# Performance work log

Hardware: AMD Instinct MI355X
Metric: run time of the kernel (lower is better)

Reference implementation:

```python
import jax, jax.numpy as jnp
import numpy as np

N_HEAD = 16
D_QK = 128
D_V = 128
D_MODEL = 2048
BATCH = 2
SEQ = 2048


def alibi_slopes(n_head):
    # standard ALiBi slopes: 2^(-8*i/n_head) for i = 1..n_head
    return jnp.asarray(2.0 ** (-8.0 * np.arange(1, n_head + 1) / n_head), dtype=jnp.float32)


def setup_inputs() -> dict:
    key = jax.random.key(0)
    k1, k2, k3, k4, k5 = jax.random.split(key, 5)
    x = jax.random.normal(k1, (BATCH, SEQ, D_MODEL), dtype=jnp.float32)
    # causal attention mask (1 = keep, 0 = masked), broadcast over heads
    causal = jnp.tril(jnp.ones((SEQ, SEQ), dtype=bool))
    attention_mask = jnp.broadcast_to(causal, (BATCH, 1, SEQ, SEQ))
    Wq = jax.random.normal(k2, (D_MODEL, N_HEAD * D_QK), dtype=jnp.float32) * (D_MODEL ** -0.5)
    Wk = jax.random.normal(k3, (D_MODEL, N_HEAD * D_QK), dtype=jnp.float32) * (D_MODEL ** -0.5)
    Wv = jax.random.normal(k4, (D_MODEL, N_HEAD * D_V), dtype=jnp.float32) * (D_MODEL ** -0.5)
    Wo = jax.random.normal(k5, (N_HEAD * D_V, D_MODEL), dtype=jnp.float32) * ((N_HEAD * D_V) ** -0.5)
    return {"x": x, "attention_mask": attention_mask, "Wq": Wq, "Wk": Wk, "Wv": Wv, "Wo": Wo}


def reference(x, attention_mask, Wq, Wk, Wv, Wo):
    B, S, _ = x.shape
    scale = D_QK ** -0.5
    q = (x @ Wq).reshape(B, S, N_HEAD, D_QK).transpose(0, 2, 1, 3)  # [B,H,S,dqk]
    k = (x @ Wk).reshape(B, S, N_HEAD, D_QK).transpose(0, 2, 1, 3)
    v = (x @ Wv).reshape(B, S, N_HEAD, D_V).transpose(0, 2, 1, 3)
    scores = jnp.einsum('bhid,bhjd->bhij', q, k) * scale  # [B,H,S,S]
    # ALiBi bias: slope_h * (j - i), negative penalty for distant past keys
    pos = jnp.arange(S, dtype=jnp.float32)
    rel = pos[None, :] - pos[:, None]  # [S,S]
    slopes = alibi_slopes(N_HEAD)
    scores = scores + slopes[None, :, None, None] * rel[None, None, :, :]
    scores = jnp.where(attention_mask, scores, jnp.float32(-jnp.inf))
    attn = jax.nn.softmax(scores, axis=-1)
    out = jnp.einsum('bhij,bhjd->bhid', attn, v)  # [B,H,S,dv]
    out = out.transpose(0, 2, 1, 3).reshape(B, S, N_HEAD * D_V)
    return out @ Wo
```

## Files before the change

### kernel.cpp

```cpp
#include <hip/hip_runtime.h>
#include <cstdint>

typedef unsigned short u16;
typedef __attribute__((ext_vector_type(4))) u16 u16x4;
typedef __attribute__((ext_vector_type(8))) u16 u16x8;
typedef __attribute__((ext_vector_type(8))) __bf16 bf16x8;
typedef __attribute__((ext_vector_type(4))) float f32x4;

#define LOG2E 1.44269504088896340736f

static __device__ __forceinline__ u16 f2bf(float f) {
  unsigned u = __builtin_bit_cast(unsigned, f);
  u += 0x7fffu + ((u >> 16) & 1u);
  return (u16)(u >> 16);
}
static __device__ __forceinline__ float bf2f(u16 v) {
  unsigned u = ((unsigned)v) << 16;
  return __builtin_bit_cast(float, u);
}


static __device__ __forceinline__ void gload16(const u16* g, u16* l) {
  __builtin_amdgcn_global_load_lds(
      (__attribute__((address_space(1))) void*)(uintptr_t)g,
      (__attribute__((address_space(3))) void*)(uintptr_t)l, 16, 0, 0);
}

static __device__ __forceinline__ bf16x8 lds_bf8(const void* p) {
  return __builtin_bit_cast(bf16x8, *(const u16x8*)p);
}

__global__ __launch_bounds__(256) void cast_x_kernel(const float* __restrict__ src,
                                                     u16* __restrict__ dst) {
  int i = (blockIdx.x * 256 + threadIdx.x) * 4;
  float4 v = *(const float4*)(src + i);
  u16x4 r = {f2bf(v.x), f2bf(v.y), f2bf(v.z), f2bf(v.w)};
  *(u16x4*)(dst + i) = r;
}

__global__ __launch_bounds__(256) void transpose_w4_kernel(const float* Wq, const float* Wk,
                                                           const float* Wv, const float* Wo,
                                                           u16* Wqt, u16* Wkt, u16* Wvt,
                                                           u16* Wot) {
  const float* src = blockIdx.z == 0 ? Wq : (blockIdx.z == 1 ? Wk : (blockIdx.z == 2 ? Wv : Wo));
  u16* dst = blockIdx.z == 0 ? Wqt : (blockIdx.z == 1 ? Wkt : (blockIdx.z == 2 ? Wvt : Wot));
  __shared__ float tile[32][33];
  const int n0 = blockIdx.x * 32, k0 = blockIdx.y * 32;
  const int tx = threadIdx.x & 31, ty = threadIdx.x >> 5;
#pragma unroll
  for (int r = 0; r < 4; ++r) {
    int row = r * 8 + ty;
    tile[row][tx] = src[(size_t)(k0 + row) * 2048 + n0 + tx];
  }
  __syncthreads();
#pragma unroll
  for (int r = 0; r < 4; ++r) {
    int row = r * 8 + ty;
    dst[(size_t)(n0 + row) * 2048 + k0 + tx] = f2bf(tile[tx][row]);
  }
}

#define QSTAGE(TILE, S)                                                              \
  do {                                                                               \
    const int bkq = (TILE) * 64;                                                     \
    u16* as_ = &lds[(S) * 16384];                                                    \
    u16* bs_ = &lds[32768 + (S) * 16384];                                            \
    gload16(pAq + bkq, as_ + tid * 8);                                               \
    gload16(pAq + bkq + (size_t)64 * 2048, as_ + 4096 + tid * 8);                    \
    gload16(pAq + bkq + (size_t)128 * 2048, as_ + 8192 + tid * 8);                   \
    gload16(pAq + bkq + (size_t)192 * 2048, as_ + 12288 + tid * 8);                  \
    gload16(pBq + bkq, bs_ + tid * 8);                                               \
    gload16(pBq + bkq + (size_t)64 * 2048, bs_ + 4096 + tid * 8);                    \
    gload16(pBq + bkq + (size_t)128 * 2048, bs_ + 8192 + tid * 8);                   \
    gload16(pBq + bkq + (size_t)192 * 2048, bs_ + 12288 + tid * 8);                  \
  } while (0)

#define QPH(S, STAGE_STMT)                                                           \
  do {                                                                               \
    const char* as_ = (const char*)&lds[(S) * 16384];                                \
    const char* bs_ = (const char*)&lds[32768 + (S) * 16384];                        \
    bf16x8 af0[8], bq0[4], af1[8], bq1[4];                                           \
    _Pragma("unroll") for (int mf = 0; mf < 8; ++mf) {                               \
      const int ar = wm * 128 + mf * 16 + l16;                                       \
      af0[mf] = lds_bf8(as_ + ((ar * 128 + lg * 16) ^ ((l16 & 7) << 4)));            \
    }                                                                                \
    _Pragma("unroll") for (int nf = 0; nf < 4; ++nf) {                               \
      const int br = wn * 64 + nf * 16 + l16;                                        \
      bq0[nf] = lds_bf8(bs_ + ((br * 128 + lg * 16) ^ ((l16 & 7) << 4)));            \
    }                                                                                \
    STAGE_STMT;                                                                      \
    asm volatile("s_barrier" ::: "memory");                                          \
    __builtin_amdgcn_s_setprio(1);                                                   \
    _Pragma("unroll") for (int mf = 0; mf < 8; ++mf)                                 \
        _Pragma("unroll") for (int nf = 0; nf < 4; ++nf) acc[mf][nf] =               \
            __builtin_amdgcn_mfma_f32_16x16x32_bf16(af0[mf], bq0[nf], acc[mf][nf], 0, 0, 0); \
    _Pragma("unroll") for (int mf = 0; mf < 8; ++mf) {                               \
      const int ar = wm * 128 + mf * 16 + l16;                                       \
      af1[mf] = lds_bf8(as_ + ((ar * 128 + (4 + lg) * 16) ^ ((l16 & 7) << 4)));      \
    }                                                                                \
    _Pragma("unroll") for (int nf = 0; nf < 4; ++nf) {                               \
      const int br = wn * 64 + nf * 16 + l16;                                        \
      bq1[nf] = lds_bf8(bs_ + ((br * 128 + (4 + lg) * 16) ^ ((l16 & 7) << 4)));      \
    }                                                                                \
    _Pragma("unroll") for (int mf = 0; mf < 8; ++mf)                                 \
        _Pragma("unroll") for (int nf = 0; nf < 4; ++nf) acc[mf][nf] =               \
            __builtin_amdgcn_mfma_f32_16x16x32_bf16(af1[mf], bq1[nf], acc[mf][nf], 0, 0, 0); \
    __builtin_amdgcn_s_setprio(0);                                                   \
    __builtin_amdgcn_sched_barrier(0);                                               \
    asm volatile("s_waitcnt vmcnt(0)\n\ts_barrier" ::: "memory");                    \
  } while (0)

__global__ __launch_bounds__(512, 1) void qkproj_kernel(const u16* __restrict__ xb,
                                                        const u16* __restrict__ Wqt,
                                                        const u16* __restrict__ Wkt,
                                                        u16* __restrict__ Qb,
                                                        u16* __restrict__ Kb) {
  const int n0g = blockIdx.y * 256;
  const u16* Bt = (n0g < 2048) ? Wqt : Wkt;
  u16* Cout = (n0g < 2048) ? Qb : Kb;
  const int m0 = blockIdx.x * 256, n0 = n0g & 2047;
  __shared__ u16 lds[65536];
  const int tid = threadIdx.x, lane = tid & 63, w = tid >> 6;
  const int wm = w >> 2, wn = w & 3;
  const int l16 = lane & 15, lg = lane >> 4;
  const int scol2 = ((tid & 7) ^ ((tid >> 3) & 7)) * 8;
  const u16* pAq = xb + (size_t)(m0 + (tid >> 3)) * 2048 + scol2;
  const u16* pBq = Bt + (size_t)(n0 + (tid >> 3)) * 2048 + scol2;

  f32x4 acc[8][4];
#pragma unroll
  for (int i = 0; i < 8; ++i)
#pragma unroll
    for (int j = 0; j < 4; ++j) acc[i][j] = f32x4{0.f, 0.f, 0.f, 0.f};

  QSTAGE(0, 0);
  asm volatile("s_waitcnt vmcnt(0)\n\ts_barrier" ::: "memory");
  for (int t = 0; t < 30; t += 2) {
    QPH(0, QSTAGE(t + 1, 1));
    QPH(1, QSTAGE(t + 2, 0));
  }
  QPH(0, QSTAGE(31, 1));
  QPH(1, (void)0);

#pragma unroll
  for (int mf = 0; mf < 8; ++mf)
#pragma unroll
    for (int nf = 0; nf < 4; ++nf)
#pragma unroll
      for (int r = 0; r < 4; ++r) {
        const int row = m0 + wm * 128 + mf * 16 + lg * 4 + r;
        const int col = n0 + wn * 64 + nf * 16 + l16;
        size_t off =
            (((size_t)(row >> 11) * 16 + (col >> 7)) * 2048 + (row & 2047)) * 128 + (col & 127);
        Cout[off] = f2bf(acc[mf][nf][r]);
      }
}

#define GSTAGE2(TILE, S)                                                             \
  do {                                                                               \
    const int bk2 = (TILE) * 64;                                                     \
    u16* as_ = &lds[(S) * 16384];                                                    \
    u16* bs_ = &lds[49152 + (S) * 8192];                                             \
    gload16(pA2 + bk2, as_ + tid * 8);                                               \
    gload16(pA2 + bk2 + (size_t)64 * 2048, as_ + 4096 + tid * 8);                    \
    gload16(pA2 + bk2 + (size_t)128 * 2048, as_ + 8192 + tid * 8);                   \
    gload16(pA2 + bk2 + (size_t)192 * 2048, as_ + 12288 + tid * 8);                  \
    gload16(pB2 + bk2, bs_ + tid * 8);                                               \
    gload16(pB2 + bk2 + (size_t)64 * 2048, bs_ + 4096 + tid * 8);                    \
  } while (0)

#define GPH2(S, STAGE_STMT, VMLIT)                                                   \
  do {                                                                               \
    const char* as_ = (const char*)&lds[(S) * 16384];                                \
    const char* bs_ = (const char*)&lds[49152 + (S) * 8192];                         \
    bf16x8 af[2][8], bq[2][2];                                                       \
    _Pragma("unroll") for (int kh = 0; kh < 2; ++kh)                                 \
        _Pragma("unroll") for (int mf = 0; mf < 8; ++mf) {                           \
      const int ar = wm * 128 + mf * 16 + l16;                                       \
      af[kh][mf] = lds_bf8(as_ + ((ar * 128 + (kh * 4 + lg) * 16) ^ ((l16 & 7) << 4))); \
    }                                                                                \
    _Pragma("unroll") for (int kh = 0; kh < 2; ++kh)                                 \
        _Pragma("unroll") for (int nf = 0; nf < 2; ++nf) {                           \
      const int br = wn * 32 + nf * 16 + l16;                                        \
      bq[kh][nf] = lds_bf8(bs_ + ((br * 128 + (kh * 4 + lg) * 16) ^ ((l16 & 7) << 4))); \
    }                                                                                \
    STAGE_STMT;                                                                      \
    asm volatile("s_barrier" ::: "memory");                                          \
    __builtin_amdgcn_s_setprio(1);                                                   \
    _Pragma("unroll") for (int kh = 0; kh < 2; ++kh)                                 \
        _Pragma("unroll") for (int mf = 0; mf < 8; ++mf)                             \
            _Pragma("unroll") for (int nf = 0; nf < 2; ++nf) acc[mf][nf] =           \
                __builtin_amdgcn_mfma_f32_16x16x32_bf16(af[kh][mf], bq[kh][nf],      \
                                                        acc[mf][nf], 0, 0, 0);      \
    __builtin_amdgcn_s_setprio(0);                                                   \
    __builtin_amdgcn_sched_barrier(0);                                               \
    asm volatile("s_waitcnt vmcnt(" #VMLIT ")\n\ts_barrier" ::: "memory");           \
  } while (0)

template <int MODE>
__device__ __forceinline__ void gemm_dp2(const u16* __restrict__ A, const u16* __restrict__ Bt,
                                         void* __restrict__ Cout, int m0, int n0) {
  __shared__ u16 lds[73728];
  const int tid = threadIdx.x, lane = tid & 63, w = tid >> 6;
  const int wm = w >> 2, wn = w & 3;
  const int l16 = lane & 15, lg = lane >> 4;
  const int scol2 = ((tid & 7) ^ ((tid >> 3) & 7)) * 8;
  const u16* pA2 = A + (size_t)(m0 + (tid >> 3)) * 2048 + scol2;
  const u16* pB2 = Bt + (size_t)(n0 + (tid >> 3)) * 2048 + scol2;

  f32x4 acc[8][2];
#pragma unroll
  for (int i = 0; i < 8; ++i)
#pragma unroll
    for (int j = 0; j < 2; ++j) acc[i][j] = f32x4{0.f, 0.f, 0.f, 0.f};

  GSTAGE2(0, 0);
  GSTAGE2(1, 1);
  asm volatile("s_waitcnt vmcnt(6)\n\ts_barrier" ::: "memory");
  for (int t = 0; t < 30; t += 3) {
    GPH2(0, GSTAGE2(t + 2, 2), 6);
    GPH2(1, GSTAGE2(t + 3, 0), 6);
    GPH2(2, GSTAGE2(t + 4, 1), 6);
  }
  GPH2(0, (void)0, 0);
  GPH2(1, (void)0, 0);

#pragma unroll
  for (int mf = 0; mf < 8; ++mf)
#pragma unroll
    for (int nf = 0; nf < 2; ++nf)
#pragma unroll
      for (int r = 0; r < 4; ++r) {
        const int row = m0 + wm * 128 + mf * 16 + lg * 4 + r;
        const int col = n0 + wn * 32 + nf * 16 + l16;
        const float v = acc[mf][nf][r];
        if constexpr (MODE == 2) {
          size_t off =
              (((size_t)(col >> 11) * 16 + (row >> 7)) * 128 + (row & 127)) * 2048 + (col & 2047);
          ((u16*)Cout)[off] = f2bf(v);
        } else {
          ((float*)Cout)[(size_t)row * 2048 + col] = v;
        }
      }
}

__global__ __launch_bounds__(512, 1) void vt_kernel(const u16* Wvt, const u16* xb, u16* Vb) {
  gemm_dp2<2>(Wvt, xb, Vb, blockIdx.x * 256, blockIdx.y * 128);
}

__global__ __launch_bounds__(512, 1) void out_kernel(const u16* OA, const u16* Wot, float* C) {
  gemm_dp2<1>(OA, Wot, C, blockIdx.x * 256, blockIdx.y * 128);
}

__global__ __launch_bounds__(256) void attn_kernel(const u16* __restrict__ Q,
                                                   const u16* __restrict__ Kg,
                                                   const u16* __restrict__ Vg,
                                                   u16* __restrict__ O,
                                                   u16* __restrict__ Opart,
                                                   float* __restrict__ Lp) {
  const int tid = threadIdx.x, lane = tid & 63, w = tid >> 6;
  const int l16 = lane & 15, lg = lane >> 4;

  const int u = blockIdx.x >> 5, bh = blockIdx.x & 31;
  int tile, st0, st1, slot = 0;
  bool multi = false;
  if (u == 0) { tile = 17; st0 = 0; st1 = 18; }
  else if (u == 1) { tile = 16; st0 = 0; st1 = 17; }
  else if (u < 30) {
    multi = true;
    const int c = u - 2, ti = c >> 1, ch = c & 1;
    tile = 31 - ti;
    const int s = tile + 1, half = (s + 1) >> 1;
    st0 = ch ? half : 0;
    st1 = ch ? s : half;
    slot = bh * 28 + c;
  } else { tile = 45 - u; st0 = 0; st1 = tile + 1; }

  const int q0 = tile * 64;
  const int h = bh & 15, b = bh >> 4;
  const float sl2 = exp2f(-0.5f * (float)(h + 1)) * LOG2E;
  const float sc2 = 0.08838834764831845f * LOG2E;

  __shared__ u16 Kl[64 * 128];
  __shared__ u16 Vl[128 * 64];
  __shared__ u16 Pl[64 * 64];

  const size_t qk_base = (size_t)bh * 2048 * 128;
  const size_t v_base = (size_t)bh * 128 * 2048;

  const u16* kgs = Kg + qk_base + (size_t)(tid >> 4) * 128 + (((tid & 15) ^ ((tid >> 4) & 7)) * 8);
  const u16* vgs = Vg + v_base + (size_t)(tid >> 3) * 2048 + (((tid & 7) ^ ((tid >> 3) & 7)) * 8);

#define STAGEKV(STX)                                                        \
  do {                                                                      \
    const int j0s = (STX)*64;                                               \
    _Pragma("unroll") for (int s = 0; s < 4; ++s) {                         \
      gload16(kgs + (size_t)(j0s + s * 16) * 128, Kl + s * 2048 + tid * 8); \
      gload16(vgs + (size_t)s * 32 * 2048 + j0s, Vl + s * 2048 + tid * 8);  \
    }                                                                       \
  } while (0)

  STAGEKV(st0);

  bf16x8 qf[4];
#pragma unroll
  for (int ks = 0; ks < 4; ++ks)
    qf[ks] = lds_bf8(&Q[qk_base + (size_t)(q0 + w * 16 + l16) * 128 + ks * 32 + lg * 8]);

  f32x4 oacc[8];
#pragma unroll
  for (int j = 0; j < 8; ++j) oacc[j] = f32x4{0.f, 0.f, 0.f, 0.f};
  float lsum0 = 0.f, lsum1 = 0.f;

  float ab4[4], rsl[4];
#pragma unroll
  for (int nf = 0; nf < 4; ++nf)
    ab4[nf] = (float)(st0 * 64 + nf * 16 - q0 - w * 16 - l16) * sl2;
#pragma unroll
  for (int r = 0; r < 4; ++r) rsl[r] = (float)(lg * 4 + r) * sl2;
  const float abinc = 64.0f * sl2;
  const int qrow = w * 16 + l16;
  const int dmaskb = lg * 4 - w * 16 - l16;

  __syncthreads();

#define ASTEP(MASKED)                                                                     \
  do {                                                                                    \
    f32x4 sacc[4];                                                                        \
    _Pragma("unroll") for (int j = 0; j < 4; ++j) sacc[j] = f32x4{0.f, 0.f, 0.f, 0.f};    \
    __builtin_amdgcn_s_setprio(1);                                                        \
    _Pragma("unroll") for (int ks = 0; ks < 4; ++ks) {                                    \
      bf16x8 kf[4];                                                                       \
      _Pragma("unroll") for (int nf = 0; nf < 4; ++nf) {                                  \
        int j = nf * 16 + l16;                                                            \
        kf[nf] = lds_bf8((char*)Kl + ((j * 256 + (ks * 32 + lg * 8) * 2) ^ ((j & 7) << 4))); \
      }                                                                                   \
      _Pragma("unroll") for (int nf = 0; nf < 4; ++nf) sacc[nf] =                         \
          __builtin_amdgcn_mfma_f32_16x16x32_bf16(kf[nf], qf[ks], sacc[nf], 0, 0, 0);     \
    }                                                                                     \
    __builtin_amdgcn_s_setprio(0);                                                        \
    _Pragma("unroll") for (int nf = 0; nf < 4; ++nf) {                                    \
      float pvv[4];                                                                       \
      _Pragma("unroll") for (int r = 0; r < 4; ++r) {                                     \
        float s2 = fmaf(sacc[nf][r], sc2, ab4[nf] + rsl[r]);                              \
        float pv = exp2f(s2);                                                             \
        if (MASKED) pv = (nf * 16 + r + dmaskb <= 0) ? pv : 0.f;                          \
        pvv[r] = pv;                                                                      \
      }                                                                                   \
      ab4[nf] += abinc;                                                                   \
      lsum0 += pvv[0] + pvv[1];                                                           \
      lsum1 += pvv[2] + pvv[3];                                                           \
      unsigned w0_, w1_;                                                                  \
      asm("v_cvt_pk_bf16_f32 %0, %1, %2" : "=v"(w0_) : "v"(pvv[0]), "v"(pvv[1]));         \
      asm("v_cvt_pk_bf16_f32 %0, %1, %2" : "=v"(w1_) : "v"(pvv[2]), "v"(pvv[3]));         \
      uint2 pw_{w0_, w1_};                                                                \
      *(uint2*)((char*)Pl + ((qrow * 128 + (nf * 16 + lg * 4) * 2) ^ ((qrow & 7) << 4))) = pw_; \
    }                                                                                     \
    __builtin_amdgcn_s_setprio(1);                                                        \
    _Pragma("unroll") for (int ks = 0; ks < 2; ++ks) {                                    \
      bf16x8 pf =                                                                         \
          lds_bf8((char*)Pl + ((qrow * 128 + (ks * 32 + lg * 8) * 2) ^ ((qrow & 7) << 4))); \
      _Pragma("unroll") for (int nf = 0; nf < 8; ++nf) {                                  \
        int d = nf * 16 + l16;                                                            \
        bf16x8 vf =                                                                       \
            lds_bf8((char*)Vl + ((d * 128 + (ks * 32 + lg * 8) * 2) ^ ((d & 7) << 4)));   \
        oacc[nf] = __builtin_amdgcn_mfma_f32_16x16x32_bf16(pf, vf, oacc[nf], 0, 0, 0);    \
      }                                                                                   \
    }                                                                                     \
    __builtin_amdgcn_s_setprio(0);                                                        \
    if (st + 1 < st1) {                                                                   \
      __syncthreads();                                                                    \
      STAGEKV(st + 1);                                                                    \
      __syncthreads();                                                                    \
    }                                                                                     \
  } while (0)

  int st = st0;
  const int bulk_end = min(st1, tile);
  for (; st < bulk_end; ++st) ASTEP(false);
  for (; st < st1; ++st) ASTEP(true);
#undef STAGEKV
#undef ASTEP

  float lr = lsum0 + lsum1;
  lr += __shfl_xor(lr, 16, 64);
  lr += __shfl_xor(lr, 32, 64);

  if (multi) {
    if (lg == 0) Lp[(size_t)slot * 64 + qrow] = lr;
#pragma unroll
    for (int r = 0; r < 4; ++r) {
      const int row = w * 16 + lg * 4 + r;
#pragma unroll
      for (int nf = 0; nf < 8; ++nf)
        Opart[((size_t)slot * 64 + row) * 128 + nf * 16 + l16] = f2bf(oacc[nf][r]);
    }
  } else {
#pragma unroll
    for (int r = 0; r < 4; ++r) {
      const float inv = 1.0f / __shfl(lr, lg * 4 + r, 64);
      const int srow = q0 + w * 16 + lg * 4 + r;
#pragma unroll
      for (int nf = 0; nf < 8; ++nf)
        O[((size_t)b * 2048 + srow) * 2048 + h * 128 + nf * 16 + l16] = f2bf(oacc[nf][r] * inv);
    }
  }
}

__global__ __launch_bounds__(256) void combine_kernel(const u16* __restrict__ Opart,
                                                      const float* __restrict__ Lp,
                                                      u16* __restrict__ O) {
  const int bx = blockIdx.x;
  const int bh = bx / 14, ti = bx % 14;
  const int tile = 31 - ti;
  const int slot0 = bh * 28 + ti * 2, slot1 = slot0 + 1;
  const int b = bh >> 4, h = bh & 15;
  const int q0 = tile * 64;
  const int tid = threadIdx.x;
  const int colg = (tid & 15) * 8, rowb = tid >> 4;
#pragma unroll
  for (int rr = 0; rr < 4; ++rr) {
    const int row = rowb + rr * 16;
    const float l0 = Lp[(size_t)slot0 * 64 + row];
    const float l1 = Lp[(size_t)slot1 * 64 + row];
    const float inv = 1.0f / (l0 + l1);
    u16x8 p0 = *(const u16x8*)&Opart[((size_t)slot0 * 64 + row) * 128 + colg];
    u16x8 p1 = *(const u16x8*)&Opart[((size_t)slot1 * 64 + row) * 128 + colg];
    u16x8 o;
#pragma unroll
    for (int e = 0; e < 8; ++e) o[e] = f2bf((bf2f(p0[e]) + bf2f(p1[e])) * inv);
    *(u16x8*)&O[((size_t)b * 2048 + q0 + row) * 2048 + h * 128 + colg] = o;
  }
}

extern "C" void kernel_launch(void* const* d_in, const int* in_sizes, int n_in, void* d_out,
                              int out_size, void* d_ws, size_t ws_size, hipStream_t stream) {
  const float* x = (const float*)d_in[0];
  const float* Wq = (const float*)d_in[2];
  const float* Wk = (const float*)d_in[3];
  const float* Wv = (const float*)d_in[4];
  const float* Wo = (const float*)d_in[5];
  char* ws = (char*)d_ws;

  const size_t MB = 1048576;
  u16* xb = (u16*)(ws);
  u16* Qb = (u16*)(ws + 16 * MB);
  u16* Kb = (u16*)(ws + 32 * MB);
  u16* Vb = (u16*)(ws + 48 * MB);
  u16* Wqt = (u16*)(ws + 64 * MB);
  u16* Wkt = (u16*)(ws + 72 * MB);
  u16* Wvt = (u16*)(ws + 80 * MB);
  u16* Wot = (u16*)(ws + 88 * MB);
  u16* OA = xb;
  u16* Opart = (u16*)(ws + 72 * MB);
  float* Lpf = (float*)(ws + 72 * MB + 896ull * 64 * 128 * 2);

  cast_x_kernel<<<8192, 256, 0, stream>>>(x, xb);
  transpose_w4_kernel<<<dim3(64, 64, 4), 256, 0, stream>>>(Wq, Wk, Wv, Wo, Wqt, Wkt, Wvt, Wot);
  qkproj_kernel<<<dim3(16, 16), 512, 0, stream>>>(xb, Wqt, Wkt, Qb, Kb);
  vt_kernel<<<dim3(8, 32), 512, 0, stream>>>(Wvt, xb, Vb);
  attn_kernel<<<dim3(1472), 256, 0, stream>>>(Qb, Kb, Vb, OA, Opart, Lpf);
  combine_kernel<<<dim3(448), 256, 0, stream>>>(Opart, Lpf, OA);
  out_kernel<<<dim3(16, 16), 512, 0, stream>>>(OA, Wot, (float*)d_out);
}
```

Baseline: 237.1 us.

## Triple-buffer A tiles in QK projection GEMM to prefetch two stages ahead

Splits the staging macro into separate A and B loads and adds a third LDS buffer for the x (A) tile, so A is fetched two k-steps ahead while B stays double-buffered. The per-phase wait becomes a partial vmcnt(4), so only the older loads must land before the barrier and more global-load latency can overlap with the MFMA work. LDS per block grows from 128KB to 160KB. The rotating buffer schedule is unrolled by hand and has to stay consistent with the wait counts.

```diff
diff --git a/kernel.cpp b/kernel.cpp
--- a/kernel.cpp
+++ b/kernel.cpp
@@ -60,25 +60,30 @@
   }
 }
 
-#define QSTAGE(TILE, S)                                                              \
+#define QSTAGE_A(TILE, S)                                                            \
   do {                                                                               \
     const int bkq = (TILE) * 64;                                                     \
     u16* as_ = &lds[(S) * 16384];                                                    \
-    u16* bs_ = &lds[32768 + (S) * 16384];                                            \
     gload16(pAq + bkq, as_ + tid * 8);                                               \
     gload16(pAq + bkq + (size_t)64 * 2048, as_ + 4096 + tid * 8);                    \
     gload16(pAq + bkq + (size_t)128 * 2048, as_ + 8192 + tid * 8);                   \
     gload16(pAq + bkq + (size_t)192 * 2048, as_ + 12288 + tid * 8);                  \
+  } while (0)
+
+#define QSTAGE_B(TILE, S)                                                            \
+  do {                                                                               \
+    const int bkq = (TILE) * 64;                                                     \
+    u16* bs_ = &lds[49152 + (S) * 16384];                                            \
     gload16(pBq + bkq, bs_ + tid * 8);                                               \
     gload16(pBq + bkq + (size_t)64 * 2048, bs_ + 4096 + tid * 8);                    \
     gload16(pBq + bkq + (size_t)128 * 2048, bs_ + 8192 + tid * 8);                   \
     gload16(pBq + bkq + (size_t)192 * 2048, bs_ + 12288 + tid * 8);                  \
   } while (0)
 
-#define QPH(S, STAGE_STMT)                                                           \
+#define QPH3(SA, SB, STAGE_STMT, VMLIT)                                              \
   do {                                                                               \
-    const char* as_ = (const char*)&lds[(S) * 16384];                                \
-    const char* bs_ = (const char*)&lds[32768 + (S) * 16384];                        \
+    const char* as_ = (const char*)&lds[(SA) * 16384];                               \
+    const char* bs_ = (const char*)&lds[49152 + (SB) * 16384];                       \
     bf16x8 af0[8], bq0[4], af1[8], bq1[4];                                           \
     _Pragma("unroll") for (int mf = 0; mf < 8; ++mf) {                               \
       const int ar = wm * 128 + mf * 16 + l16;                                       \
@@ -107,7 +112,7 @@
             __builtin_amdgcn_mfma_f32_16x16x32_bf16(af1[mf], bq1[nf], acc[mf][nf], 0, 0, 0); \
     __builtin_amdgcn_s_setprio(0);                                                   \
     __builtin_amdgcn_sched_barrier(0);                                               \
-    asm volatile("s_waitcnt vmcnt(0)\n\ts_barrier" ::: "memory");                    \
+    asm volatile("s_waitcnt vmcnt(" #VMLIT ")\n\ts_barrier" ::: "memory");           \
   } while (0)
 
 __global__ __launch_bounds__(512, 1) void qkproj_kernel(const u16* __restrict__ xb,
@@ -119,7 +124,7 @@
   const u16* Bt = (n0g < 2048) ? Wqt : Wkt;
   u16* Cout = (n0g < 2048) ? Qb : Kb;
   const int m0 = blockIdx.x * 256, n0 = n0g & 2047;
-  __shared__ u16 lds[65536];
+  __shared__ u16 lds[81920];
   const int tid = threadIdx.x, lane = tid & 63, w = tid >> 6;
   const int wm = w >> 2, wn = w & 3;
   const int l16 = lane & 15, lg = lane >> 4;
@@ -133,14 +138,20 @@
 #pragma unroll
     for (int j = 0; j < 4; ++j) acc[i][j] = f32x4{0.f, 0.f, 0.f, 0.f};
 
-  QSTAGE(0, 0);
-  asm volatile("s_waitcnt vmcnt(0)\n\ts_barrier" ::: "memory");
-  for (int t = 0; t < 30; t += 2) {
-    QPH(0, QSTAGE(t + 1, 1));
-    QPH(1, QSTAGE(t + 2, 0));
-  }
-  QPH(0, QSTAGE(31, 1));
-  QPH(1, (void)0);
+  QSTAGE_A(0, 0);
+  QSTAGE_B(0, 0);
+  QSTAGE_A(1, 1);
+  asm volatile("s_waitcnt vmcnt(4)\n\ts_barrier" ::: "memory");
+  for (int t = 0; t < 30; t += 6) {
+    QPH3(0, 0, QSTAGE_B(t + 1, 1); QSTAGE_A(t + 2, 2), 4);
+    QPH3(1, 1, QSTAGE_B(t + 2, 0); QSTAGE_A(t + 3, 0), 4);
+    QPH3(2, 0, QSTAGE_B(t + 3, 1); QSTAGE_A(t + 4, 1), 4);
+    QPH3(0, 1, QSTAGE_B(t + 4, 0); QSTAGE_A(t + 5, 2), 4);
+    QPH3(1, 0, QSTAGE_B(t + 5, 1); QSTAGE_A(t + 6, 0), 4);
+    QPH3(2, 1, QSTAGE_B(t + 6, 0); QSTAGE_A(t + 7, 1), 4);
+  }
+  QPH3(0, 0, QSTAGE_B(31, 1), 0);
+  QPH3(1, 1, (void)0, 0);
 
 #pragma unroll
   for (int mf = 0; mf < 8; ++mf)
```

New measurement: 238.1 us. No clear change (+0.4%).
